# Performance work log

Hardware: AMD Instinct MI355X
Metric: run time of the kernel (lower is better)

## Reference

```python
import jax, jax.numpy as jnp
import numpy as np

N_EL = 19        # electrodes per graph (hardcoded in module)
N_EDGES = 342    # 19*18 directed edges per graph, no self-loops
N_GRAPHS = 1800
C_IN = 128
C_OUT = 128


def setup_inputs() -> dict:
    key = jax.random.key(0)
    k1, k2, k3 = jax.random.split(key, 3)
    N = N_GRAPHS * N_EL
    x = jax.random.normal(k1, (N, C_IN), dtype=jnp.float32)
    # block-structured edge_index: same 342-edge pattern in every 19-node graph
    src_b, dst_b = np.nonzero(~np.eye(N_EL, dtype=bool))  # all i != j pairs
    offs = (np.arange(N_GRAPHS) * N_EL)[:, None]
    src = (src_b[None, :] + offs).reshape(-1)
    dst = (dst_b[None, :] + offs).reshape(-1)
    edge_index = jnp.asarray(np.stack([src, dst]), dtype=jnp.int32)  # [2, E]
    # learnable params: edge_weights init 'ones'; GraphConv lin_rel (bias) + lin_root (no bias)
    edge_weights = jnp.ones((N_EDGES,), dtype=jnp.float32)
    W_rel = jax.random.normal(k2, (C_OUT, C_IN), dtype=jnp.float32) * 0.05
    b_rel = jnp.zeros((C_OUT,), dtype=jnp.float32)
    W_root = jax.random.normal(k3, (C_OUT, C_IN), dtype=jnp.float32) * 0.05
    return {"x": x, "edge_index": edge_index, "edge_weights": edge_weights,
            "W_rel": W_rel, "b_rel": b_rel, "W_root": W_root}


def reference(x, edge_index, edge_weights, W_rel, b_rel, W_root):
    # repeat per-graph edge weights across all graphs (torch .repeat == jnp.tile)
    E = edge_index.shape[1]
    rep = jnp.tile(edge_weights, E // edge_weights.shape[0])          # [E]
    src, dst = edge_index[0], edge_index[1]
    # GraphConv message passing: gather source features, scale, scatter-add to targets
    msg = x[src] * rep[:, None]                                       # [E, C_in]
    agg = jax.ops.segment_sum(msg, dst, num_segments=x.shape[0])      # [N, C_in]
    # out = lin_rel(agg) + lin_root(x)
    return agg @ W_rel.T + b_rel + x @ W_root.T
```

## Files before the change

kernel.cpp:

```cpp
#include <hip/hip_runtime.h>
#include <hip/hip_bf16.h>

#define EPG 342
#define LDX 136
#define LDT 72

typedef short short8 __attribute__((ext_vector_type(8)));
typedef float f32x4  __attribute__((ext_vector_type(4)));

static __device__ __forceinline__ unsigned int f2bf(float f) {
    unsigned int u = __float_as_uint(f);
    return (u + 0x7fffu + ((u >> 16) & 1u)) >> 16;
}
static __device__ __forceinline__ int pk2(float lo, float hi) {
    return (int)(f2bf(lo) | (f2bf(hi) << 16));
}

__global__ __launch_bounds__(256) void conv_w(
    const float* __restrict__ Wrel, const float* __restrict__ Wroot,
    unsigned short* __restrict__ wsW)
{
    int tid = blockIdx.x * 256 + threadIdx.x;
    const float* src = (tid < 4096) ? (Wrel + tid * 4)
                                    : (Wroot + (tid - 4096) * 4);
    float4 v = *(const float4*)src;
    int2 w; w.x = pk2(v.x, v.y); w.y = pk2(v.z, v.w);
    *(int2*)&wsW[tid * 4] = w;
}

__global__ __launch_bounds__(256) void fused(
    const float* __restrict__ x,
    const float* __restrict__ ew,
    const unsigned short* __restrict__ wsW,
    const float* __restrict__ brel,
    float* __restrict__ out)
{
    __shared__ __align__(16) unsigned short Xs[64 * LDX];
    __shared__ __align__(16) unsigned short T1T[128 * LDT];

    const int t    = threadIdx.x;
    const int lane = t & 63;
    const int wv   = t >> 6;
    const int g0   = blockIdx.x * 2;
    const int lrow = lane & 15;
    const int kq   = (lane >> 4) * 8;

    const float4* xg = (const float4*)(x + (size_t)g0 * 19 * 128);
    float4 xc[5];
    #pragma unroll
    for (int q = 0; q < 5; ++q) { int i = t + q * 256; if (i < 1216) xc[q] = xg[i]; }

    short8 wf[4][4];
    #pragma unroll
    for (int nl = 0; nl < 4; ++nl) {
        int col = (wv + nl * 4) * 16 + lrow;
        #pragma unroll
        for (int ks = 0; ks < 4; ++ks)
            wf[nl][ks] = *(const short8*)&wsW[(size_t)col * 128 + ks * 32 + kq];
    }

    short8 aa[2];
    #pragma unroll
    for (int mt = 0; mt < 2; ++mt) {
        int m = mt * 16 + lrow;
        union { short8 s; unsigned short h[8]; } u;
        #pragma unroll
        for (int j = 0; j < 8; ++j) {
            int k = kq + j;
            unsigned short hv = 0;
            if (m < 19 && k < 19 && k != m)
                hv = (unsigned short)f2bf(ew[k * 18 + m - (m > k)]);
            u.h[j] = hv;
        }
        aa[mt] = u.s;
    }

    const float b0 = brel[wv * 16 + lrow];
    const float b1 = brel[(wv + 4) * 16 + lrow];

    {
        int4 z = {0, 0, 0, 0};
        for (int i = t; i < 416; i += 256) {
            int r = i >> 4, c = i & 15;
            int g = (r >= 13); int lr = 19 + r - g * 13;
            *(int4*)&Xs[(g * 32 + lr) * LDX + c * 8] = z;
        }
    }
    #pragma unroll
    for (int q = 0; q < 5; ++q) {
        int i = t + q * 256;
        if (i < 1216) {
            int row = i >> 5, c4 = i & 31;
            int g = (row >= 19); int lr = row - g * 19;
            float4 v = xc[q];
            int2 w; w.x = pk2(v.x, v.y); w.y = pk2(v.z, v.w);
            *(int2*)&Xs[(g * 32 + lr) * LDX + c4 * 4] = w;
        }
    }
    __syncthreads();

    f32x4 acc[4][4];
    #pragma unroll
    for (int mt = 0; mt < 4; ++mt)
        #pragma unroll
        for (int nl = 0; nl < 4; ++nl) acc[mt][nl] = (f32x4){0.f, 0.f, 0.f, 0.f};

    #pragma unroll
    for (int ks = 0; ks < 4; ++ks) {
        short8 af[4];
        #pragma unroll
        for (int mt = 0; mt < 4; ++mt)
            af[mt] = *(const short8*)&Xs[(mt * 16 + lrow) * LDX + ks * 32 + kq];
        #pragma unroll
        for (int mt = 0; mt < 4; ++mt)
            #pragma unroll
            for (int nl = 0; nl < 4; ++nl)
                acc[mt][nl] = __builtin_amdgcn_mfma_f32_16x16x32_bf16(
                    af[mt], wf[nl][ks], acc[mt][nl], 0, 0, 0);
    }

    #pragma unroll
    for (int mt = 0; mt < 4; ++mt)
        #pragma unroll
        for (int nl = 0; nl < 2; ++nl) {
            int col = (wv + nl * 4) * 16 + lrow;
            int r0  = mt * 16 + (lane >> 4) * 4;
            f32x4 a = acc[mt][nl];
            int2 w; w.x = pk2(a[0], a[1]); w.y = pk2(a[2], a[3]);
            *(int2*)&T1T[col * LDT + r0] = w;
        }
    __syncthreads();

    #pragma unroll
    for (int g = 0; g < 2; ++g) {
        #pragma unroll
        for (int mt = 0; mt < 2; ++mt) {
            #pragma unroll
            for (int nl = 0; nl < 2; ++nl) {
                int col = (wv + nl * 4) * 16 + lrow;
                short8 bb = *(const short8*)&T1T[col * LDT + g * 32 + kq];
                f32x4 c = acc[g * 2 + mt][nl + 2];
                c = __builtin_amdgcn_mfma_f32_16x16x32_bf16(aa[mt], bb, c, 0, 0, 0);
                int m0 = mt * 16 + (lane >> 4) * 4;
                float bias = nl ? b1 : b0;
                float* og = out + (size_t)(g0 + g) * 19 * 128 + col;
                #pragma unroll
                for (int r = 0; r < 4; ++r) {
                    int m = m0 + r;
                    if (m < 19) og[m * 128] = c[r] + bias;
                }
            }
        }
    }
}

extern "C" void kernel_launch(void* const* d_in, const int* in_sizes, int n_in,
                              void* d_out, int out_size, void* d_ws, size_t ws_size,
                              hipStream_t stream) {
    const float* x     = (const float*)d_in[0];
    const float* ew    = (const float*)d_in[2];
    const float* Wrel  = (const float*)d_in[3];
    const float* brel  = (const float*)d_in[4];
    const float* Wroot = (const float*)d_in[5];
    float* out = (float*)d_out;

    unsigned short* wsW = (unsigned short*)d_ws;

    const int E_total  = in_sizes[1] / 2;
    const int n_graphs = E_total / EPG;

    conv_w<<<32, 256, 0, stream>>>(Wrel, Wroot, wsW);
    fused<<<n_graphs / 2, 256, 0, stream>>>(x, ew, wsW, brel, out);
}
```

Before: 97.37 us.

## Pack three graphs contiguously per block with block-diagonal adjacency MFMA

Each block now handles 57 contiguous node rows (three graphs) instead of two graphs padded to 32 rows each. The 64-row MFMA tile wastes fewer padded rows, and the aggregation becomes a 64x64 block-diagonal adjacency matmul with two k-steps per tile. This cuts the block count by a third and improves MFMA utilisation. In exchange each thread keeps more adjacency fragments and x registers, which may lower occupancy, and the launch assumes the graph count is divisible by three.

```diff
diff --git a/kernel.cpp b/kernel.cpp
--- a/kernel.cpp
+++ b/kernel.cpp
@@ -2,6 +2,8 @@
 #include <hip/hip_bf16.h>
 
 #define EPG 342
+#define GPB 3
+#define RPB 57
 #define LDX 136
 #define LDT 72
 
@@ -41,14 +43,14 @@
     const int t    = threadIdx.x;
     const int lane = t & 63;
     const int wv   = t >> 6;
-    const int g0   = blockIdx.x * 2;
     const int lrow = lane & 15;
     const int kq   = (lane >> 4) * 8;
+    const int r0   = blockIdx.x * RPB;
 
-    const float4* xg = (const float4*)(x + (size_t)g0 * 19 * 128);
-    float4 xc[5];
+    const float4* xg = (const float4*)(x + (size_t)r0 * 128);
+    float4 xc[8];
     #pragma unroll
-    for (int q = 0; q < 5; ++q) { int i = t + q * 256; if (i < 1216) xc[q] = xg[i]; }
+    for (int q = 0; q < 8; ++q) { int i = t + q * 256; if (i < 1824) xc[q] = xg[i]; }
 
     short8 wf[4][4];
     #pragma unroll
@@ -59,42 +61,43 @@
             wf[nl][ks] = *(const short8*)&wsW[(size_t)col * 128 + ks * 32 + kq];
     }
 
-    short8 aa[2];
+    short8 aa[4][2];
     #pragma unroll
-    for (int mt = 0; mt < 2; ++mt) {
-        int m = mt * 16 + lrow;
-        union { short8 s; unsigned short h[8]; } u;
+    for (int mt = 0; mt < 4; ++mt) {
+        int m  = mt * 16 + lrow;
+        int gm = m / 19, lm = m - gm * 19;
         #pragma unroll
-        for (int j = 0; j < 8; ++j) {
-            int k = kq + j;
-            unsigned short hv = 0;
-            if (m < 19 && k < 19 && k != m)
-                hv = (unsigned short)f2bf(ew[k * 18 + m - (m > k)]);
-            u.h[j] = hv;
+        for (int ks = 0; ks < 2; ++ks) {
+            union { short8 s; unsigned short h[8]; } u;
+            #pragma unroll
+            for (int j = 0; j < 8; ++j) {
+                int k  = ks * 32 + kq + j;
+                int gk = k / 19, lk = k - gk * 19;
+                unsigned short hv = 0;
+                if (m < RPB && k < RPB && gm == gk && lm != lk)
+                    hv = (unsigned short)f2bf(ew[lk * 18 + lm - (lm > lk)]);
+                u.h[j] = hv;
+            }
+            aa[mt][ks] = u.s;
         }
-        aa[mt] = u.s;
     }
 
     const float b0 = brel[wv * 16 + lrow];
     const float b1 = brel[(wv + 4) * 16 + lrow];
 
-    {
+    if (t < 112) {
         int4 z = {0, 0, 0, 0};
-        for (int i = t; i < 416; i += 256) {
-            int r = i >> 4, c = i & 15;
-            int g = (r >= 13); int lr = 19 + r - g * 13;
-            *(int4*)&Xs[(g * 32 + lr) * LDX + c * 8] = z;
-        }
+        int r = RPB + (t >> 4), c = t & 15;
+        *(int4*)&Xs[r * LDX + c * 8] = z;
     }
     #pragma unroll
-    for (int q = 0; q < 5; ++q) {
+    for (int q = 0; q < 8; ++q) {
         int i = t + q * 256;
-        if (i < 1216) {
+        if (i < 1824) {
             int row = i >> 5, c4 = i & 31;
-            int g = (row >= 19); int lr = row - g * 19;
             float4 v = xc[q];
             int2 w; w.x = pk2(v.x, v.y); w.y = pk2(v.z, v.w);
-            *(int2*)&Xs[(g * 32 + lr) * LDX + c4 * 4] = w;
+            *(int2*)&Xs[row * LDX + c4 * 4] = w;
         }
     }
     __syncthreads();
@@ -124,31 +127,31 @@
         #pragma unroll
         for (int nl = 0; nl < 2; ++nl) {
             int col = (wv + nl * 4) * 16 + lrow;
-            int r0  = mt * 16 + (lane >> 4) * 4;
+            int k0  = mt * 16 + (lane >> 4) * 4;
             f32x4 a = acc[mt][nl];
             int2 w; w.x = pk2(a[0], a[1]); w.y = pk2(a[2], a[3]);
-            *(int2*)&T1T[col * LDT + r0] = w;
+            *(int2*)&T1T[col * LDT + k0] = w;
         }
     __syncthreads();
 
     #pragma unroll
-    for (int g = 0; g < 2; ++g) {
+    for (int mt = 0; mt < 4; ++mt) {
         #pragma unroll
-        for (int mt = 0; mt < 2; ++mt) {
+        for (int nl = 0; nl < 2; ++nl) {
+            int col = (wv + nl * 4) * 16 + lrow;
+            f32x4 c = acc[mt][nl + 2];
             #pragma unroll
-            for (int nl = 0; nl < 2; ++nl) {
-                int col = (wv + nl * 4) * 16 + lrow;
-                short8 bb = *(const short8*)&T1T[col * LDT + g * 32 + kq];
-                f32x4 c = acc[g * 2 + mt][nl + 2];
-                c = __builtin_amdgcn_mfma_f32_16x16x32_bf16(aa[mt], bb, c, 0, 0, 0);
-                int m0 = mt * 16 + (lane >> 4) * 4;
-                float bias = nl ? b1 : b0;
-                float* og = out + (size_t)(g0 + g) * 19 * 128 + col;
-                #pragma unroll
-                for (int r = 0; r < 4; ++r) {
-                    int m = m0 + r;
-                    if (m < 19) og[m * 128] = c[r] + bias;
-                }
+            for (int ks = 0; ks < 2; ++ks) {
+                short8 bb = *(const short8*)&T1T[col * LDT + ks * 32 + kq];
+                c = __builtin_amdgcn_mfma_f32_16x16x32_bf16(aa[mt][ks], bb, c, 0, 0, 0);
+            }
+            int m0 = mt * 16 + (lane >> 4) * 4;
+            float bias = nl ? b1 : b0;
+            float* og = out + (size_t)r0 * 128 + col;
+            #pragma unroll
+            for (int r = 0; r < 4; ++r) {
+                int m = m0 + r;
+                if (m < RPB) og[m * 128] = c[r] + bias;
             }
         }
     }
@@ -168,7 +171,8 @@
 
     const int E_total  = in_sizes[1] / 2;
     const int n_graphs = E_total / EPG;
+    const int n_blocks = n_graphs / GPB;
 
     conv_w<<<32, 256, 0, stream>>>(Wrel, Wroot, wsW);
-    fused<<<n_graphs / 2, 256, 0, stream>>>(x, ew, wsW, brel, out);
+    fused<<<n_blocks, 256, 0, stream>>>(x, ew, wsW, brel, out);
 }
```

Measured after the change: 102.9 us. 1.06x slower.
